# Optimization experiments

Hardware: AMD Instinct MI355X
Metric: run time of the kernel (lower is better)

Reference implementation:

```python
import jax, jax.numpy as jnp
import numpy as np

D_MODEL = 1024
NUM_HEADS = 16
D_K = D_MODEL // NUM_HEADS


def setup_inputs() -> dict:
    key = jax.random.key(0)
    ks = jax.random.split(key, 11)
    B, S = 2, 2048
    scale = 1.0 / np.sqrt(D_MODEL)
    inp = {
        "query": jax.random.normal(ks[0], (B, S, D_MODEL), jnp.float32),
        "key": jax.random.normal(ks[1], (B, S, D_MODEL), jnp.float32),
        "value": jax.random.normal(ks[2], (B, S, D_MODEL), jnp.float32),
        "Wq": jax.random.normal(ks[3], (D_MODEL, D_MODEL), jnp.float32) * scale,
        "bq": jnp.zeros((D_MODEL,), jnp.float32),
        "Wk": jax.random.normal(ks[4], (D_MODEL, D_MODEL), jnp.float32) * scale,
        "bk": jnp.zeros((D_MODEL,), jnp.float32),
        "Wv": jax.random.normal(ks[5], (D_MODEL, D_MODEL), jnp.float32) * scale,
        "bv": jnp.zeros((D_MODEL,), jnp.float32),
        "Wo": jax.random.normal(ks[6], (D_MODEL, D_MODEL), jnp.float32) * scale,
        "bo": jnp.zeros((D_MODEL,), jnp.float32),
    }
    return inp


def _split_heads(x):
    B, S, _ = x.shape
    return x.reshape(B, S, NUM_HEADS, D_K).transpose(0, 2, 1, 3)  # [B,H,S,d_k]


def reference(query, key, value, Wq, bq, Wk, bk, Wv, bv, Wo, bo):
    # Linear projections (torch Linear: x @ W.T + b)
    q = _split_heads(query @ Wq.T + bq)
    k = _split_heads(key @ Wk.T + bk)
    v = _split_heads(value @ Wv.T + bv)
    scores = jnp.einsum("bhqd,bhkd->bhqk", q, k) / jnp.sqrt(jnp.float32(D_K))
    probs = jax.nn.softmax(scores, axis=-1)
    out = jnp.einsum("bhqk,bhkd->bhqd", probs, v)  # [B,H,S,d_k]
    B, H, S, _ = out.shape
    out = out.transpose(0, 2, 1, 3).reshape(B, S, D_MODEL)
    return out @ Wo.T + bo
```

## Files before the change

kernel.cpp:

```cpp
#include <hip/hip_runtime.h>

#define D_MODEL 1024
#define NHEADS  16
#define DK      64
#define SEQ     2048
#define NBATCH  2
#define MTOT    (NBATCH * SEQ)

typedef _Float16 f16;
typedef _Float16 f16x4 __attribute__((ext_vector_type(4)));
typedef _Float16 f16x8 __attribute__((ext_vector_type(8)));
typedef float    f32x4 __attribute__((ext_vector_type(4)));
typedef float    f32x16 __attribute__((ext_vector_type(16)));

#define LOG2E 1.44269504088896340736f

__global__ __launch_bounds__(256) void cvt_f32_to_f16(
    const float* __restrict__ q, const float* __restrict__ k, const float* __restrict__ v,
    const float* __restrict__ wq, const float* __restrict__ wk,
    const float* __restrict__ wv, const float* __restrict__ wo,
    f16* __restrict__ qf, f16* __restrict__ kf, f16* __restrict__ vf,
    f16* __restrict__ wqh, f16* __restrict__ wkh, f16* __restrict__ wvh, f16* __restrict__ woh)
{
    const int z = blockIdx.y;
    const float* src; f16* dst; int n4;
    if (z == 0)      { src = q;  dst = qf;  n4 = MTOT * D_MODEL / 4; }
    else if (z == 1) { src = k;  dst = kf;  n4 = MTOT * D_MODEL / 4; }
    else if (z == 2) { src = v;  dst = vf;  n4 = MTOT * D_MODEL / 4; }
    else if (z == 3) { src = wq; dst = wqh; n4 = D_MODEL * D_MODEL / 4; }
    else if (z == 4) { src = wk; dst = wkh; n4 = D_MODEL * D_MODEL / 4; }
    else if (z == 5) { src = wv; dst = wvh; n4 = D_MODEL * D_MODEL / 4; }
    else             { src = wo; dst = woh; n4 = D_MODEL * D_MODEL / 4; }
    for (int i = blockIdx.x * 256 + threadIdx.x; i < n4; i += gridDim.x * 256) {
        float4 t = ((const float4*)src)[i];
        f16x4 o = {(f16)t.x, (f16)t.y, (f16)t.z, (f16)t.w};
        ((f16x4*)dst)[i] = o;
    }
}

__device__ __forceinline__ void gemm128_core(
    const f16* __restrict__ A, const f16* __restrict__ Wm,
    int m0, int n0, int kbeg, int kend, f32x16 (&acc)[2][2])
{
    __shared__ __align__(16) f16 As[4096];
    __shared__ __align__(16) f16 Bs[4096];

    const int t    = threadIdx.x;
    const int lane = t & 63;
    const int w    = t >> 6;
    const int l31  = lane & 31, kg = lane >> 5;
    const int wr   = w >> 1,    wc = w & 1;

    size_t offA[2], offB[2];
#pragma unroll
    for (int jj = 0; jj < 2; ++jj) {
        int s  = (w * 2 + jj) * 64 + lane;
        int ko = s >> 7, m = s & 127;
        offA[jj] = (size_t)(m0 + m) * D_MODEL + ko * 8;
        offB[jj] = (size_t)(n0 + m) * D_MODEL + ko * 8;
    }
    const int jb = __builtin_amdgcn_readfirstlane(w * 1024);

#pragma unroll
    for (int i = 0; i < 2; ++i)
#pragma unroll
        for (int j = 0; j < 2; ++j)
#pragma unroll
            for (int r = 0; r < 16; ++r) acc[i][j][r] = 0.f;

    auto* ldsA = (__attribute__((address_space(3))) f16*)As;
    auto* ldsB = (__attribute__((address_space(3))) f16*)Bs;

    for (int k0 = kbeg; k0 < kend; k0 += 32) {
#pragma unroll
        for (int jj = 0; jj < 2; ++jj) {
            __builtin_amdgcn_global_load_lds(
                (const __attribute__((address_space(1))) void*)(A + offA[jj] + k0),
                (__attribute__((address_space(3))) void*)(ldsA + jb + jj * 512),
                16, 0, 0);
            __builtin_amdgcn_global_load_lds(
                (const __attribute__((address_space(1))) void*)(Wm + offB[jj] + k0),
                (__attribute__((address_space(3))) void*)(ldsB + jb + jj * 512),
                16, 0, 0);
        }
        __syncthreads();

#pragma unroll
        for (int step = 0; step < 2; ++step) {
            const int kk = kg + 2 * step;
            f16x8 aF[2], bF[2];
#pragma unroll
            for (int ti = 0; ti < 2; ++ti) {
                aF[ti] = *(const f16x8*)&As[(kk * 128 + wr * 64 + ti * 32 + l31) * 8];
                bF[ti] = *(const f16x8*)&Bs[(kk * 128 + wc * 64 + ti * 32 + l31) * 8];
            }
#pragma unroll
            for (int ti = 0; ti < 2; ++ti)
#pragma unroll
                for (int tj = 0; tj < 2; ++tj)
                    acc[ti][tj] = __builtin_amdgcn_mfma_f32_32x32x16_f16(
                        aF[ti], bF[tj], acc[ti][tj], 0, 0, 0);
        }
        __syncthreads();
    }
}

__global__ __launch_bounds__(256, 3) void qkv_gemm(
    const f16* __restrict__ Qf, const f16* __restrict__ Kf, const f16* __restrict__ Vf,
    const f16* __restrict__ Wqh, const f16* __restrict__ Wkh, const f16* __restrict__ Wvh,
    const float* __restrict__ bq, const float* __restrict__ bk, const float* __restrict__ bv,
    f16* __restrict__ Qh, f16* __restrict__ Kh, f16* __restrict__ Vt)
{
    const int z = blockIdx.z;
    const f16*   A    = z == 0 ? Qf  : z == 1 ? Kf  : Vf;
    const f16*   Wm   = z == 0 ? Wqh : z == 1 ? Wkh : Wvh;
    const float* bias = z == 0 ? bq  : z == 1 ? bk  : bv;

    const int m0 = blockIdx.x * 128, n0 = blockIdx.y * 128;
    f32x16 acc[2][2];
    gemm128_core(A, Wm, m0, n0, 0, D_MODEL, acc);

    const int t = threadIdx.x, lane = t & 63, w = t >> 6;
    const int l31 = lane & 31, kg = lane >> 5;
    const int wr = w >> 1, wc = w & 1;

    if (z < 2) {
        f16* Out = z == 0 ? Qh : Kh;
        const float sc = z == 0 ? 0.125f * LOG2E : 1.0f;
#pragma unroll
        for (int tj = 0; tj < 2; ++tj) {
            const int col = n0 + wc * 64 + tj * 32 + l31;
            const float bc = bias[col];
#pragma unroll
            for (int ti = 0; ti < 2; ++ti)
#pragma unroll
                for (int r = 0; r < 16; ++r) {
                    const int row = m0 + wr * 64 + ti * 32 + (r & 3) + 8 * (r >> 2) + 4 * kg;
                    Out[(size_t)row * D_MODEL + col] = (f16)((acc[ti][tj][r] + bc) * sc);
                }
        }
    } else {
#pragma unroll
        for (int tj = 0; tj < 2; ++tj) {
            const int col = n0 + wc * 64 + tj * 32 + l31;
            const float bc = bias[col];
            const int h = col >> 6, d = col & 63;
#pragma unroll
            for (int ti = 0; ti < 2; ++ti)
#pragma unroll
                for (int r = 0; r < 16; ++r) {
                    const int row = m0 + wr * 64 + ti * 32 + (r & 3) + 8 * (r >> 2) + 4 * kg;
                    const int bb = row >> 11, s = row & (SEQ - 1);
                    Vt[(size_t)((bb * NHEADS + h) * DK + d) * SEQ + s] = (f16)(acc[ti][tj][r] + bc);
                }
        }
    }
}

__global__ __launch_bounds__(256, 3) void oproj_splitk(
    const f16* __restrict__ A, const f16* __restrict__ Wm,
    float* __restrict__ P0, float* __restrict__ P1)
{
    const int z = blockIdx.z;
    const int m0 = blockIdx.x * 128, n0 = blockIdx.y * 128;
    f32x16 acc[2][2];
    gemm128_core(A, Wm, m0, n0, z * 512, z * 512 + 512, acc);

    float* Out = z == 0 ? P0 : P1;
    const int t = threadIdx.x, lane = t & 63, w = t >> 6;
    const int l31 = lane & 31, kg = lane >> 5;
    const int wr = w >> 1, wc = w & 1;
#pragma unroll
    for (int tj = 0; tj < 2; ++tj) {
        const int col = n0 + wc * 64 + tj * 32 + l31;
#pragma unroll
        for (int ti = 0; ti < 2; ++ti)
#pragma unroll
            for (int r = 0; r < 16; ++r) {
                const int row = m0 + wr * 64 + ti * 32 + (r & 3) + 8 * (r >> 2) + 4 * kg;
                Out[(size_t)row * D_MODEL + col] = acc[ti][tj][r];
            }
    }
}

__global__ __launch_bounds__(256) void reduce_bias(
    const float* __restrict__ P0, const float* __restrict__ P1,
    const float* __restrict__ bias, float* __restrict__ Out)
{
    const int n4 = MTOT * D_MODEL / 4;
    for (int i = blockIdx.x * 256 + threadIdx.x; i < n4; i += gridDim.x * 256) {
        float4 a = ((const float4*)P0)[i];
        float4 b = ((const float4*)P1)[i];
        float4 c = ((const float4*)bias)[i & 255];
        float4 o = {a.x + b.x + c.x, a.y + b.y + c.y,
                    a.z + b.z + c.z, a.w + b.w + c.w};
        ((float4*)Out)[i] = o;
    }
}

__global__ __launch_bounds__(256, 4) void mha_mfma_v7(
    const f16* __restrict__ Qh, const f16* __restrict__ Kh,
    const f16* __restrict__ Vt, f16* __restrict__ Op, float* __restrict__ sp)
{
    __shared__ __align__(16) f16 Ks[4096];
    __shared__ __align__(16) f16 Vc[4096];
    __shared__ __align__(16) f16 Ps[128 * 68];

    const int t    = threadIdx.x;
    const int w    = t >> 6;
    const int lane = t & 63;
    const int quad = lane >> 4, l15 = lane & 15;

    const int bh = blockIdx.x, qt = blockIdx.y, half = blockIdx.z;
    const int b  = bh >> 4,    h  = bh & 15;
    const int q0 = qt * 128;

    f16x8 aQ[2][2];
#pragma unroll
    for (int s = 0; s < 2; ++s)
#pragma unroll
        for (int c = 0; c < 2; ++c)
            aQ[s][c] = *(const f16x8*)&Qh[
                (size_t)(b * SEQ + q0 + w * 32 + s * 16 + l15) * D_MODEL
                + h * DK + c * 32 + quad * 8];

    const f16* gK[2]; const f16* gV[2]; int ldst[2];
#pragma unroll
    for (int jj = 0; jj < 2; ++jj) {
        const int kc = w * 2 + jj;
        gK[jj] = Kh + (size_t)(b * SEQ + lane) * D_MODEL + h * DK + kc * 8;
        gV[jj] = Vt + (size_t)(bh * DK + lane) * SEQ + kc * 8;
        ldst[jj] = __builtin_amdgcn_readfirstlane(kc * 512);
    }
    auto* ldsK = (__attribute__((address_space(3))) f16*)Ks;
    auto* ldsV = (__attribute__((address_space(3))) f16*)Vc;

    const f16x8 onesB = {(f16)1.f, (f16)1.f, (f16)1.f, (f16)1.f,
                         (f16)1.f, (f16)1.f, (f16)1.f, (f16)1.f};

    f32x4 o[2][4];
#pragma unroll
    for (int s = 0; s < 2; ++s)
#pragma unroll
        for (int j = 0; j < 4; ++j) o[s][j] = (f32x4){0.f, 0.f, 0.f, 0.f};
    f32x4 sacc[2] = {(f32x4){0.f, 0.f, 0.f, 0.f}, (f32x4){0.f, 0.f, 0.f, 0.f}};

    const int kt0 = half * (SEQ / 128);
    for (int kt = kt0; kt < kt0 + SEQ / 128; ++kt) {
#pragma unroll
        for (int jj = 0; jj < 2; ++jj) {
            __builtin_amdgcn_global_load_lds(
                (const __attribute__((address_space(1))) void*)(gK[jj] + (size_t)kt * 64 * D_MODEL),
                (__attribute__((address_space(3))) void*)(ldsK + ldst[jj]), 16, 0, 0);
            __builtin_amdgcn_global_load_lds(
                (const __attribute__((address_space(1))) void*)(gV[jj] + kt * 64),
                (__attribute__((address_space(3))) void*)(ldsV + ldst[jj]), 16, 0, 0);
        }
        __syncthreads();

        f16x8 bK[4][2], bV[4][2];
#pragma unroll
        for (int f = 0; f < 4; ++f)
#pragma unroll
            for (int c = 0; c < 2; ++c) {
                const int slot = ((c * 4 + quad) * 64 + f * 16 + l15) * 8;
                bK[f][c] = *(const f16x8*)&Ks[slot];
                bV[f][c] = *(const f16x8*)&Vc[slot];
            }

#pragma unroll
        for (int s = 0; s < 2; ++s) {
            f32x4 sc[4];
#pragma unroll
            for (int f = 0; f < 4; ++f) {
                f32x4 a = (f32x4){0.f, 0.f, 0.f, 0.f};
                a = __builtin_amdgcn_mfma_f32_16x16x32_f16(aQ[s][0], bK[f][0], a, 0, 0, 0);
                a = __builtin_amdgcn_mfma_f32_16x16x32_f16(aQ[s][1], bK[f][1], a, 0, 0, 0);
                sc[f] = a;
            }

#pragma unroll
            for (int f = 0; f < 4; ++f)
#pragma unroll
                for (int r = 0; r < 4; ++r)
                    sc[f][r] = __builtin_exp2f(sc[f][r]);

#pragma unroll
            for (int f = 0; f < 4; ++f)
#pragma unroll
                for (int r = 0; r < 4; ++r)
                    Ps[(w * 32 + s * 16 + quad * 4 + r) * 68 + f * 16 + l15] = (f16)sc[f][r];

            f16x8 aP[2];
#pragma unroll
            for (int c = 0; c < 2; ++c) {
                const int off = (w * 32 + s * 16 + l15) * 68 + c * 32 + quad * 8;
                f16x4 lo = *(const f16x4*)&Ps[off];
                f16x4 hi = *(const f16x4*)&Ps[off + 4];
                aP[c] = __builtin_shufflevector(lo, hi, 0, 1, 2, 3, 4, 5, 6, 7);
            }

#pragma unroll
            for (int j = 0; j < 4; ++j) {
                o[s][j] = __builtin_amdgcn_mfma_f32_16x16x32_f16(aP[0], bV[j][0], o[s][j], 0, 0, 0);
                o[s][j] = __builtin_amdgcn_mfma_f32_16x16x32_f16(aP[1], bV[j][1], o[s][j], 0, 0, 0);
            }
            sacc[s] = __builtin_amdgcn_mfma_f32_16x16x32_f16(aP[0], onesB, sacc[s], 0, 0, 0);
            sacc[s] = __builtin_amdgcn_mfma_f32_16x16x32_f16(aP[1], onesB, sacc[s], 0, 0, 0);
        }
        __syncthreads();
    }

#pragma unroll
    for (int s = 0; s < 2; ++s)
#pragma unroll
        for (int r = 0; r < 4; ++r) {
            const int qrow = q0 + w * 32 + s * 16 + quad * 4 + r;
            const size_t base = ((size_t)(half * 32 + bh) * SEQ + qrow) * DK;
#pragma unroll
            for (int j = 0; j < 4; ++j)
                Op[base + j * 16 + l15] = (f16)o[s][j][r];
            if (l15 == 0)
                sp[(size_t)(half * 32 + bh) * SEQ + qrow] = sacc[s][r];
        }
}

__global__ __launch_bounds__(256) void mha_combine(
    const f16* __restrict__ Op, const float* __restrict__ sp,
    f16* __restrict__ ATh)
{
    const int gid = blockIdx.x * 256 + threadIdx.x;
    const int d4 = gid & 15;
    const int q  = (gid >> 4) & (SEQ - 1);
    const int bh = gid >> 15;
    const int b = bh >> 4, h = bh & 15;

    const size_t i0 = ((size_t)bh * SEQ + q) * DK + d4 * 4;
    const size_t i1 = ((size_t)(32 + bh) * SEQ + q) * DK + d4 * 4;
    f16x4 a = *(const f16x4*)&Op[i0];
    f16x4 c = *(const f16x4*)&Op[i1];
    const float inv = 1.f / (sp[(size_t)bh * SEQ + q] + sp[(size_t)(32 + bh) * SEQ + q]);
    f16x4 r;
#pragma unroll
    for (int m = 0; m < 4; ++m)
        r[m] = (f16)(((float)a[m] + (float)c[m]) * inv);
    *(f16x4*)&ATh[((size_t)(b * SEQ + q)) * D_MODEL + h * DK + d4 * 4] = r;
}

extern "C" void kernel_launch(void* const* d_in, const int* in_sizes, int n_in,
                              void* d_out, int out_size, void* d_ws, size_t ws_size,
                              hipStream_t stream)
{
    const float* query = (const float*)d_in[0];
    const float* key   = (const float*)d_in[1];
    const float* value = (const float*)d_in[2];
    const float* Wq    = (const float*)d_in[3];
    const float* bq    = (const float*)d_in[4];
    const float* Wk    = (const float*)d_in[5];
    const float* bk    = (const float*)d_in[6];
    const float* Wv    = (const float*)d_in[7];
    const float* bv    = (const float*)d_in[8];
    const float* Wo    = (const float*)d_in[9];
    const float* bo    = (const float*)d_in[10];
    float* out = (float*)d_out;

    f16* Qf  = (f16*)d_ws;
    f16* Kf  = Qf  + (size_t)MTOT * D_MODEL;
    f16* Vf  = Kf  + (size_t)MTOT * D_MODEL;
    f16* Wqh = Vf  + (size_t)MTOT * D_MODEL;
    f16* Wkh = Wqh + (size_t)D_MODEL * D_MODEL;
    f16* Wvh = Wkh + (size_t)D_MODEL * D_MODEL;
    f16* Woh = Wvh + (size_t)D_MODEL * D_MODEL;
    f16* Qh  = Woh + (size_t)D_MODEL * D_MODEL;
    f16* Kh  = Qh  + (size_t)MTOT * D_MODEL;
    f16* Vt  = Kh  + (size_t)MTOT * D_MODEL;
    f16* ATh = Vt  + (size_t)MTOT * D_MODEL;

    f16*   Op = Qf;
    float* sp = (float*)(Vf + (size_t)1024 * 1024);
    float* P0 = (float*)Qf;
    float* P1 = (float*)Qh;

    cvt_f32_to_f16<<<dim3(1024, 7), 256, 0, stream>>>(
        query, key, value, Wq, Wk, Wv, Wo, Qf, Kf, Vf, Wqh, Wkh, Wvh, Woh);

    qkv_gemm<<<dim3(MTOT / 128, D_MODEL / 128, 3), 256, 0, stream>>>(
        Qf, Kf, Vf, Wqh, Wkh, Wvh, bq, bk, bv, Qh, Kh, Vt);

    mha_mfma_v7<<<dim3(NBATCH * NHEADS, SEQ / 128, 2), 256, 0, stream>>>(
        Qh, Kh, Vt, Op, sp);

    mha_combine<<<dim3(MTOT * D_MODEL / 4 / 256), 256, 0, stream>>>(Op, sp, ATh);

    oproj_splitk<<<dim3(MTOT / 128, D_MODEL / 128, 2), 256, 0, stream>>>(ATh, Woh, P0, P1);

    reduce_bias<<<dim3(1024), 256, 0, stream>>>(P0, P1, bo, out);
}
```

Before: 264.6 us.

## Split attention key range three ways and raise occupancy with smaller P tile

```diff
diff --git a/kernel.cpp b/kernel.cpp
--- a/kernel.cpp
+++ b/kernel.cpp
@@ -198,20 +198,20 @@
     }
 }
 
-__global__ __launch_bounds__(256, 4) void mha_mfma_v7(
+__global__ __launch_bounds__(256, 6) void mha_mfma_v8(
     const f16* __restrict__ Qh, const f16* __restrict__ Kh,
     const f16* __restrict__ Vt, f16* __restrict__ Op, float* __restrict__ sp)
 {
     __shared__ __align__(16) f16 Ks[4096];
     __shared__ __align__(16) f16 Vc[4096];
-    __shared__ __align__(16) f16 Ps[128 * 68];
+    __shared__ __align__(16) f16 Ps[64 * 68];
 
     const int t    = threadIdx.x;
     const int w    = t >> 6;
     const int lane = t & 63;
     const int quad = lane >> 4, l15 = lane & 15;
 
-    const int bh = blockIdx.x, qt = blockIdx.y, half = blockIdx.z;
+    const int bh = blockIdx.x, qt = blockIdx.y, third = blockIdx.z;
     const int b  = bh >> 4,    h  = bh & 15;
     const int q0 = qt * 128;
 
@@ -245,8 +245,9 @@
         for (int j = 0; j < 4; ++j) o[s][j] = (f32x4){0.f, 0.f, 0.f, 0.f};
     f32x4 sacc[2] = {(f32x4){0.f, 0.f, 0.f, 0.f}, (f32x4){0.f, 0.f, 0.f, 0.f}};
 
-    const int kt0 = half * (SEQ / 128);
-    for (int kt = kt0; kt < kt0 + SEQ / 128; ++kt) {
+    const int kt0   = third * 11;
+    const int ktend = (third == 2) ? 32 : kt0 + 11;
+    for (int kt = kt0; kt < ktend; ++kt) {
 #pragma unroll
         for (int jj = 0; jj < 2; ++jj) {
             __builtin_amdgcn_global_load_lds(
@@ -289,12 +290,12 @@
             for (int f = 0; f < 4; ++f)
 #pragma unroll
                 for (int r = 0; r < 4; ++r)
-                    Ps[(w * 32 + s * 16 + quad * 4 + r) * 68 + f * 16 + l15] = (f16)sc[f][r];
+                    Ps[(w * 16 + quad * 4 + r) * 68 + f * 16 + l15] = (f16)sc[f][r];
 
             f16x8 aP[2];
 #pragma unroll
             for (int c = 0; c < 2; ++c) {
-                const int off = (w * 32 + s * 16 + l15) * 68 + c * 32 + quad * 8;
+                const int off = (w * 16 + l15) * 68 + c * 32 + quad * 8;
                 f16x4 lo = *(const f16x4*)&Ps[off];
                 f16x4 hi = *(const f16x4*)&Ps[off + 4];
                 aP[c] = __builtin_shufflevector(lo, hi, 0, 1, 2, 3, 4, 5, 6, 7);
@@ -316,12 +317,12 @@
 #pragma unroll
         for (int r = 0; r < 4; ++r) {
             const int qrow = q0 + w * 32 + s * 16 + quad * 4 + r;
-            const size_t base = ((size_t)(half * 32 + bh) * SEQ + qrow) * DK;
+            const size_t base = ((size_t)(third * 32 + bh) * SEQ + qrow) * DK;
 #pragma unroll
             for (int j = 0; j < 4; ++j)
                 Op[base + j * 16 + l15] = (f16)o[s][j][r];
             if (l15 == 0)
-                sp[(size_t)(half * 32 + bh) * SEQ + qrow] = sacc[s][r];
+                sp[(size_t)(third * 32 + bh) * SEQ + qrow] = sacc[s][r];
         }
 }
 
@@ -335,15 +336,20 @@
     const int bh = gid >> 15;
     const int b = bh >> 4, h = bh & 15;
 
-    const size_t i0 = ((size_t)bh * SEQ + q) * DK + d4 * 4;
-    const size_t i1 = ((size_t)(32 + bh) * SEQ + q) * DK + d4 * 4;
-    f16x4 a = *(const f16x4*)&Op[i0];
-    f16x4 c = *(const f16x4*)&Op[i1];
-    const float inv = 1.f / (sp[(size_t)bh * SEQ + q] + sp[(size_t)(32 + bh) * SEQ + q]);
+    float acc[4] = {0.f, 0.f, 0.f, 0.f};
+    float ssum = 0.f;
+#pragma unroll
+    for (int tpart = 0; tpart < 3; ++tpart) {
+        const size_t idx = ((size_t)(tpart * 32 + bh) * SEQ + q) * DK + d4 * 4;
+        f16x4 a = *(const f16x4*)&Op[idx];
+#pragma unroll
+        for (int m = 0; m < 4; ++m) acc[m] += (float)a[m];
+        ssum += sp[(size_t)(tpart * 32 + bh) * SEQ + q];
+    }
+    const float inv = 1.f / ssum;
     f16x4 r;
 #pragma unroll
-    for (int m = 0; m < 4; ++m)
-        r[m] = (f16)(((float)a[m] + (float)c[m]) * inv);
+    for (int m = 0; m < 4; ++m) r[m] = (f16)(acc[m] * inv);
     *(f16x4*)&ATh[((size_t)(b * SEQ + q)) * D_MODEL + h * DK + d4 * 4] = r;
 }
 
@@ -377,7 +383,7 @@
     f16* ATh = Vt  + (size_t)MTOT * D_MODEL;
 
     f16*   Op = Qf;
-    float* sp = (float*)(Vf + (size_t)1024 * 1024);
+    float* sp = (float*)Wqh;
     float* P0 = (float*)Qf;
     float* P1 = (float*)Qh;
 
@@ -387,7 +393,7 @@
     qkv_gemm<<<dim3(MTOT / 128, D_MODEL / 128, 3), 256, 0, stream>>>(
         Qf, Kf, Vf, Wqh, Wkh, Wvh, bq, bk, bv, Qh, Kh, Vt);
 
-    mha_mfma_v7<<<dim3(NBATCH * NHEADS, SEQ / 128, 2), 256, 0, stream>>>(
+    mha_mfma_v8<<<dim3(NBATCH * NHEADS, SEQ / 128, 3), 256, 0, stream>>>(
         Qh, Kh, Vt, Op, sp);
 
     mha_combine<<<dim3(MTOT * D_MODEL / 4 / 256), 256, 0, stream>>>(Op, sp, ATh);
```

Result: slower. 440.4 us (+66.4%).
